# Kernel optimization log

Measured on AMD Instinct MI355X. Metric: run time of the kernel, lower is better.

The kernel has to match this reference:

```python
import jax, jax.numpy as jnp
import numpy as np
import math

V_ORDER = 22
N_ORDER = 22
HID = 128
MAX_ABS = 0.99
LOG_F0_MIN = math.log(80.0)
LOG_F0_MAX = math.log(1000.0)
OUT = 1 + V_ORDER + 1 + N_ORDER + 1 + HID  # 175


def setup_inputs() -> dict:
    key = jax.random.key(0)
    k1, k2, k3 = jax.random.split(key, 3)
    B, F, D = 32, 1000, 1024
    h = jax.random.normal(k1, (B, F, D), jnp.float32)
    W = jax.random.normal(k2, (OUT, D), jnp.float32) * 0.02
    b = jax.random.normal(k3, (OUT,), jnp.float32) * 0.1
    return {"h": h, "W": W, "b": b}


def _logits2biquads(logits):
    # conj representation: logits (..., 2) -> monic biquad coeffs (..., 3)
    mag = jax.nn.sigmoid(logits[..., 0]) * MAX_ABS
    phase = jax.nn.sigmoid(logits[..., 1]) * jnp.pi
    a1 = -2.0 * mag * jnp.cos(phase)
    a2 = mag * mag
    return jnp.stack([jnp.ones_like(a1), a1, a2], axis=-1)


def _biquads2lpc(biquads):
    # biquads: (..., S, 3) monic sections -> full LPC poly coeffs (..., 2S)
    # sequentially convolve the S second-order sections (b0 == 1 exactly)
    S = biquads.shape[-2]
    L = 2 * S + 1
    poly = jnp.zeros(biquads.shape[:-2] + (L,), biquads.dtype).at[..., 0].set(1.0)

    def shift(p, n):
        pad = [(0, 0)] * (p.ndim - 1) + [(n, 0)]
        return jnp.pad(p, pad)[..., :L]

    for i in range(S):  # small fixed S (=11), fully vectorized over batch/frames
        a1 = biquads[..., i, 1:2]
        a2 = biquads[..., i, 2:3]
        poly = poly + shift(poly, 1) * a1 + shift(poly, 2) * a2
    return poly[..., 1:]  # drop leading 1


def reference(h, W, b):
    B, F, _ = h.shape
    y = jnp.einsum('bfd,od->bfo', h, W) + b  # backbone out_linear
    idx = np.cumsum([1, V_ORDER, 1, N_ORDER, 1])
    f0_l, v_lpc_l, v_gain_l, n_lpc_l, n_gain_l, h_feat = jnp.split(y, idx, axis=-1)
    f0 = jnp.exp(jax.nn.sigmoid(f0_l[..., 0]) * (LOG_F0_MAX - LOG_F0_MIN) + LOG_F0_MIN)
    voice_lpc = _biquads2lpc(_logits2biquads(v_lpc_l.reshape(B, F, -1, 2)))
    noise_lpc = _biquads2lpc(_logits2biquads(n_lpc_l.reshape(B, F, -1, 2)))
    voice_gain = jnp.exp(v_gain_l[..., 0])
    noise_gain = jnp.exp(n_gain_l[..., 0])
    # flat version of (f0, (h,), (voice_gain, voice_lpc), (noise_gain, noise_lpc), ())
    return (f0, h_feat, voice_gain, voice_lpc, noise_gain, noise_lpc)
```

## Files before the change

### kernel.cpp

```cpp
#include <hip/hip_runtime.h>
#include <math.h>

#define D_DIM  1024
#define OUT_N  175
#define HID_N  128
#define BM     64
#define BK     32
#define NT     (D_DIM / BK)
#define LDK    40
#define NFRAG  11
#define FRAG_STRIDE 512

#define V_OFF   1
#define VG_OFF  23
#define N_OFF   24
#define NG_OFF  46
#define HF_OFF  47

#define LOG_F0_MIN 4.3820266346738812f
#define LOG_F0_MAX 6.9077552789821368f
#define PI_F       3.14159265358979323846f

typedef __attribute__((ext_vector_type(8))) short s16x8;
typedef __attribute__((ext_vector_type(4))) short s16x4;
typedef __attribute__((ext_vector_type(4))) float f32x4;

static __device__ __forceinline__ short f2bf(float f) {
    unsigned u = __float_as_uint(f);
    unsigned r = (u + 0x7fffu + ((u >> 16) & 1u)) >> 16;
    return (short)r;
}
static __device__ __forceinline__ float bf2f(short s) {
    return __uint_as_float(((unsigned)(unsigned short)s) << 16);
}

__global__ __launch_bounds__(64) void build_wfrag(
    const float* __restrict__ W, short* __restrict__ whiF, short* __restrict__ wloF)
{
    const int ft   = blockIdx.x;
    const int j    = ft >> 5;
    const int t    = ft & 31;
    const int lane = threadIdx.x;
    const int n    = 16 * j + (lane & 15);
    const int k    = 32 * t + (lane >> 4) * 8;

    float v[8];
    if (n < OUT_N) {
        float4 p0 = *(const float4*)(W + (size_t)n * D_DIM + k);
        float4 p1 = *(const float4*)(W + (size_t)n * D_DIM + k + 4);
        v[0] = p0.x; v[1] = p0.y; v[2] = p0.z; v[3] = p0.w;
        v[4] = p1.x; v[5] = p1.y; v[6] = p1.z; v[7] = p1.w;
    } else {
        #pragma unroll
        for (int e = 0; e < 8; ++e) v[e] = 0.f;
    }
    s16x8 hv, lv;
    #pragma unroll
    for (int e = 0; e < 8; ++e) {
        short hb = f2bf(v[e]);
        hv[e] = hb;
        lv[e] = f2bf(v[e] - bf2f(hb));
    }
    const size_t off = ((size_t)ft * 64 + lane) * 8;
    *(s16x8*)(whiF + off) = hv;
    *(s16x8*)(wloF + off) = lv;
}

#define SMEM_BYTES 12544

__global__ __launch_bounds__(512, 4) void glottal_main(
    const float* __restrict__ h, const short* __restrict__ whiF,
    const short* __restrict__ wloF, const float* __restrict__ bias,
    float* __restrict__ out, int R)
{
    __shared__ __align__(16) char smem[SMEM_BYTES];
    short* AhiS = (short*)smem;
    short* AloS = AhiS + BM * LDK;
    float (*yS)[49] = (float (*)[49])smem;

    const int tid  = threadIdx.x;
    const int r0   = blockIdx.x * BM;

    const int lane = tid & 63;
    const int wid  = tid >> 6;
    const int c    = lane & 15;
    const int kg   = lane >> 4;
    const int mh   = wid >> 2;
    const int jg   = wid & 3;
    const int jcnt = (jg < 3) ? 3 : 2;

    const int rA  = tid >> 3;
    const int kqA = (tid & 7) << 2;
    int gA = r0 + rA; if (gA >= R) gA = R - 1;
    const float* hP = h + (size_t)gA * D_DIM + kqA;

    const short* bhP[3];
    const short* blP[3];
    #pragma unroll
    for (int jj = 0; jj < 3; ++jj) {
        int j = 3 * jg + jj; if (j > NFRAG - 1) j = NFRAG - 1;
        bhP[jj] = whiF + (size_t)j * NT * FRAG_STRIDE + lane * 8;
        blP[jj] = wloF + (size_t)j * NT * FRAG_STRIDE + lane * 8;
    }

    f32x4 acc[2][3];
    #pragma unroll
    for (int mm = 0; mm < 2; ++mm)
        #pragma unroll
        for (int jj = 0; jj < 3; ++jj) acc[mm][jj] = f32x4{0.f, 0.f, 0.f, 0.f};

    float4 aC = *(const float4*)(hP);
    s16x8 bhC[3], blC[3];
    #pragma unroll
    for (int jj = 0; jj < 3; ++jj) if (jj < jcnt) {
        bhC[jj] = *(const s16x8*)(bhP[jj]);
        blC[jj] = *(const s16x8*)(blP[jj]);
    }

    for (int t = 0; t < NT; ++t) {
        {
            s16x4 hv, lv;
            hv.x = f2bf(aC.x); lv.x = f2bf(aC.x - bf2f(hv.x));
            hv.y = f2bf(aC.y); lv.y = f2bf(aC.y - bf2f(hv.y));
            hv.z = f2bf(aC.z); lv.z = f2bf(aC.z - bf2f(hv.z));
            hv.w = f2bf(aC.w); lv.w = f2bf(aC.w - bf2f(hv.w));
            *(s16x4*)(AhiS + rA * LDK + kqA) = hv;
            *(s16x4*)(AloS + rA * LDK + kqA) = lv;
        }
        __syncthreads();

        float4 aN;
        s16x8 bhN[3], blN[3];
        const bool more = (t + 1 < NT);
        if (more) {
            aN = *(const float4*)(hP + (t + 1) * BK);
            #pragma unroll
            for (int jj = 0; jj < 3; ++jj) if (jj < jcnt) {
                bhN[jj] = *(const s16x8*)(bhP[jj] + (size_t)(t + 1) * FRAG_STRIDE);
                blN[jj] = *(const s16x8*)(blP[jj] + (size_t)(t + 1) * FRAG_STRIDE);
            }
        }

        s16x8 ah[2], al[2];
        #pragma unroll
        for (int mm = 0; mm < 2; ++mm) {
            const int ro = (32 * mh + 16 * mm + c) * LDK + kg * 8;
            ah[mm] = *(const s16x8*)(AhiS + ro);
            al[mm] = *(const s16x8*)(AloS + ro);
        }

        #pragma unroll
        for (int jj = 0; jj < 3; ++jj) if (jj < jcnt) {
            #pragma unroll
            for (int mm = 0; mm < 2; ++mm) {
                acc[mm][jj] = __builtin_amdgcn_mfma_f32_16x16x32_bf16(ah[mm], bhC[jj], acc[mm][jj], 0, 0, 0);
                acc[mm][jj] = __builtin_amdgcn_mfma_f32_16x16x32_bf16(ah[mm], blC[jj], acc[mm][jj], 0, 0, 0);
                acc[mm][jj] = __builtin_amdgcn_mfma_f32_16x16x32_bf16(al[mm], bhC[jj], acc[mm][jj], 0, 0, 0);
            }
        }
        __syncthreads();

        if (more) {
            aC = aN;
            #pragma unroll
            for (int jj = 0; jj < 3; ++jj) if (jj < jcnt) {
                bhC[jj] = bhN[jj];
                blC[jj] = blN[jj];
            }
        }
    }

    const size_t Rz = (size_t)R;

    #pragma unroll
    for (int jj = 0; jj < 3; ++jj) if (jj < jcnt) {
        const int j   = 3 * jg + jj;
        const int col = 16 * j + c;
        const float bb = (col < OUT_N) ? bias[col] : 0.f;
        #pragma unroll
        for (int mm = 0; mm < 2; ++mm) {
            const int rb = 32 * mh + 16 * mm + (kg << 2);
            if (col >= HF_OFF && col < OUT_N) {
                #pragma unroll
                for (int r = 0; r < 4; ++r) {
                    int gr = r0 + rb + r;
                    if (gr < R)
                        out[Rz + (size_t)gr * HID_N + (col - HF_OFF)] = acc[mm][jj][r] + bb;
                }
            } else if (col < HF_OFF) {
                #pragma unroll
                for (int r = 0; r < 4; ++r)
                    yS[rb + r][col] = acc[mm][jj][r] + bb;
            }
        }
    }
    __syncthreads();

    if (tid < 2 * BM) {
        const int rr   = tid >> 1;
        const int half = tid & 1;
        const int gr   = r0 + rr;
        if (gr < R) {
            const float* yrow = yS[rr];

            if (half == 0) {
                float s = 1.f / (1.f + expf(-yrow[0]));
                out[gr] = expf(s * (LOG_F0_MAX - LOG_F0_MIN) + LOG_F0_MIN);
            }

            const int lbase = half ? N_OFF  : V_OFF;
            const int gidx  = half ? NG_OFF : VG_OFF;
            float*    gout  = out + (half ? Rz * 152 : Rz * 129);
            float*    lout  = out + (half ? Rz * 153 : Rz * 130);

            gout[gr] = expf(yrow[gidx]);

            float poly[23];
            poly[0] = 1.f;
            #pragma unroll
            for (int j = 1; j < 23; ++j) poly[j] = 0.f;

            #pragma unroll
            for (int i = 0; i < 11; ++i) {
                float l0  = yrow[lbase + 2 * i];
                float l1  = yrow[lbase + 2 * i + 1];
                float mag = 0.99f / (1.f + expf(-l0));
                float ph  = PI_F   / (1.f + expf(-l1));
                float a1  = -2.f * mag * cosf(ph);
                float a2  = mag * mag;
                #pragma unroll
                for (int j = 22; j >= 2; --j)
                    poly[j] = fmaf(a1, poly[j - 1], fmaf(a2, poly[j - 2], poly[j]));
                poly[1] = fmaf(a1, poly[0], poly[1]);
            }

            #pragma unroll
            for (int j = 0; j < 22; ++j)
                lout[(size_t)gr * 22 + j] = poly[j + 1];
        }
    }
}

extern "C" void kernel_launch(void* const* d_in, const int* in_sizes, int n_in,
                              void* d_out, int out_size, void* d_ws, size_t ws_size,
                              hipStream_t stream) {
    const float* h    = (const float*)d_in[0];
    const float* W    = (const float*)d_in[1];
    const float* bias = (const float*)d_in[2];
    float* out        = (float*)d_out;

    const int R = in_sizes[0] / D_DIM;
    const int blocks = (R + BM - 1) / BM;

    short* whiF = (short*)d_ws;
    short* wloF = whiF + (size_t)NFRAG * NT * FRAG_STRIDE;

    build_wfrag<<<NFRAG * NT, 64, 0, stream>>>(W, whiF, wloF);
    glottal_main<<<blocks, 512, 0, stream>>>(h, whiF, wloF, bias, out, R);
}
```

Before: 226.2 us.

## Stage 128-wide K chunks with register prefetch and fewer waves per block

The main GEMM kernel now runs 4 waves per block instead of 8. Each wave covers all 64 rows for its column fragments, so every W fragment loaded is reused across four M tiles. The activation tile is staged in LDS as 128-wide K chunks (four 32-wide sub-tiles), and the next chunk is prefetched into registers one chunk ahead. This cuts barriers from two per 32-wide K step to two per 128-wide chunk and halves W fragment traffic per block. In exchange each thread holds more registers (12 accumulators and 8 prefetched float4s), LDS use per block rises, and fewer waves are resident per CU.

```diff
diff --git a/kernel.cpp b/kernel.cpp
--- a/kernel.cpp
+++ b/kernel.cpp
@@ -5,11 +5,13 @@
 #define OUT_N  175
 #define HID_N  128
 #define BM     64
-#define BK     32
-#define NT     (D_DIM / BK)
-#define LDK    40
+#define NT     32
 #define NFRAG  11
 #define FRAG_STRIDE 512
+#define CH     128
+#define NCH    (D_DIM / CH)
+#define TPC    4
+#define SUBT   2576
 
 #define V_OFF   1
 #define VG_OFF  23
@@ -66,16 +68,16 @@
     *(s16x8*)(wloF + off) = lv;
 }
 
-#define SMEM_BYTES 12544
-
-__global__ __launch_bounds__(512, 4) void glottal_main(
+#define SMEM_BYTES (2 * TPC * SUBT * 2)
+
+__global__ __launch_bounds__(256, 2) void glottal_main(
     const float* __restrict__ h, const short* __restrict__ whiF,
     const short* __restrict__ wloF, const float* __restrict__ bias,
     float* __restrict__ out, int R)
 {
     __shared__ __align__(16) char smem[SMEM_BYTES];
     short* AhiS = (short*)smem;
-    short* AloS = AhiS + BM * LDK;
+    short* AloS = AhiS + TPC * SUBT;
     float (*yS)[49] = (float (*)[49])smem;
 
     const int tid  = threadIdx.x;
@@ -85,14 +87,13 @@
     const int wid  = tid >> 6;
     const int c    = lane & 15;
     const int kg   = lane >> 4;
-    const int mh   = wid >> 2;
-    const int jg   = wid & 3;
+    const int jg   = wid;
     const int jcnt = (jg < 3) ? 3 : 2;
 
-    const int rA  = tid >> 3;
-    const int kqA = (tid & 7) << 2;
-    int gA = r0 + rA; if (gA >= R) gA = R - 1;
-    const float* hP = h + (size_t)gA * D_DIM + kqA;
+    const int srow = tid >> 5;
+    const int scf  = tid & 31;
+    const int st4  = scf >> 3;
+    const int sko  = (scf & 7) << 2;
 
     const short* bhP[3];
     const short* blP[3];
@@ -103,70 +104,99 @@
         blP[jj] = wloF + (size_t)j * NT * FRAG_STRIDE + lane * 8;
     }
 
-    f32x4 acc[2][3];
-    #pragma unroll
-    for (int mm = 0; mm < 2; ++mm)
+    f32x4 acc[4][3];
+    #pragma unroll
+    for (int mm = 0; mm < 4; ++mm)
         #pragma unroll
         for (int jj = 0; jj < 3; ++jj) acc[mm][jj] = f32x4{0.f, 0.f, 0.f, 0.f};
 
-    float4 aC = *(const float4*)(hP);
-    s16x8 bhC[3], blC[3];
-    #pragma unroll
-    for (int jj = 0; jj < 3; ++jj) if (jj < jcnt) {
-        bhC[jj] = *(const s16x8*)(bhP[jj]);
-        blC[jj] = *(const s16x8*)(blP[jj]);
-    }
-
-    for (int t = 0; t < NT; ++t) {
-        {
-            s16x4 hv, lv;
-            hv.x = f2bf(aC.x); lv.x = f2bf(aC.x - bf2f(hv.x));
-            hv.y = f2bf(aC.y); lv.y = f2bf(aC.y - bf2f(hv.y));
-            hv.z = f2bf(aC.z); lv.z = f2bf(aC.z - bf2f(hv.z));
-            hv.w = f2bf(aC.w); lv.w = f2bf(aC.w - bf2f(hv.w));
-            *(s16x4*)(AhiS + rA * LDK + kqA) = hv;
-            *(s16x4*)(AloS + rA * LDK + kqA) = lv;
+    const float* hP[8];
+    #pragma unroll
+    for (int i = 0; i < 8; ++i) {
+        int gr = r0 + srow + 8 * i; if (gr >= R) gr = R - 1;
+        hP[i] = h + (size_t)gr * D_DIM + scf * 4;
+    }
+
+    float4 sA[8];
+
+    #pragma unroll
+    for (int i = 0; i < 8; ++i) sA[i] = *(const float4*)(hP[i]);
+    #pragma unroll
+    for (int i = 0; i < 8; ++i) {
+        const int base = st4 * SUBT + (srow + 8 * i) * 40 + sko;
+        s16x4 hv, lv;
+        hv.x = f2bf(sA[i].x); lv.x = f2bf(sA[i].x - bf2f(hv.x));
+        hv.y = f2bf(sA[i].y); lv.y = f2bf(sA[i].y - bf2f(hv.y));
+        hv.z = f2bf(sA[i].z); lv.z = f2bf(sA[i].z - bf2f(hv.z));
+        hv.w = f2bf(sA[i].w); lv.w = f2bf(sA[i].w - bf2f(hv.w));
+        *(s16x4*)(AhiS + base) = hv;
+        *(s16x4*)(AloS + base) = lv;
+    }
+    #pragma unroll
+    for (int i = 0; i < 8; ++i) sA[i] = *(const float4*)(hP[i] + CH);
+    __syncthreads();
+
+    for (int ch = 0; ch < NCH; ++ch) {
+        s16x8 bhC[3], blC[3];
+        const int tg0 = ch * TPC;
+        #pragma unroll
+        for (int jj = 0; jj < 3; ++jj) if (jj < jcnt) {
+            bhC[jj] = *(const s16x8*)(bhP[jj] + (size_t)tg0 * FRAG_STRIDE);
+            blC[jj] = *(const s16x8*)(blP[jj] + (size_t)tg0 * FRAG_STRIDE);
+        }
+        #pragma unroll
+        for (int t4 = 0; t4 < TPC; ++t4) {
+            s16x8 ah[4], al[4];
+            #pragma unroll
+            for (int mm = 0; mm < 4; ++mm) {
+                const int off = t4 * SUBT + (16 * mm + c) * 40 + kg * 8;
+                ah[mm] = *(const s16x8*)(AhiS + off);
+                al[mm] = *(const s16x8*)(AloS + off);
+            }
+            s16x8 bhN[3], blN[3];
+            if (t4 < TPC - 1) {
+                #pragma unroll
+                for (int jj = 0; jj < 3; ++jj) if (jj < jcnt) {
+                    bhN[jj] = *(const s16x8*)(bhP[jj] + (size_t)(tg0 + t4 + 1) * FRAG_STRIDE);
+                    blN[jj] = *(const s16x8*)(blP[jj] + (size_t)(tg0 + t4 + 1) * FRAG_STRIDE);
+                }
+            }
+            #pragma unroll
+            for (int jj = 0; jj < 3; ++jj) if (jj < jcnt) {
+                #pragma unroll
+                for (int mm = 0; mm < 4; ++mm) {
+                    acc[mm][jj] = __builtin_amdgcn_mfma_f32_16x16x32_bf16(ah[mm], bhC[jj], acc[mm][jj], 0, 0, 0);
+                    acc[mm][jj] = __builtin_amdgcn_mfma_f32_16x16x32_bf16(ah[mm], blC[jj], acc[mm][jj], 0, 0, 0);
+                    acc[mm][jj] = __builtin_amdgcn_mfma_f32_16x16x32_bf16(al[mm], bhC[jj], acc[mm][jj], 0, 0, 0);
+                }
+            }
+            if (t4 < TPC - 1) {
+                #pragma unroll
+                for (int jj = 0; jj < 3; ++jj) if (jj < jcnt) {
+                    bhC[jj] = bhN[jj]; blC[jj] = blN[jj];
+                }
+            }
         }
         __syncthreads();
 
-        float4 aN;
-        s16x8 bhN[3], blN[3];
-        const bool more = (t + 1 < NT);
-        if (more) {
-            aN = *(const float4*)(hP + (t + 1) * BK);
-            #pragma unroll
-            for (int jj = 0; jj < 3; ++jj) if (jj < jcnt) {
-                bhN[jj] = *(const s16x8*)(bhP[jj] + (size_t)(t + 1) * FRAG_STRIDE);
-                blN[jj] = *(const s16x8*)(blP[jj] + (size_t)(t + 1) * FRAG_STRIDE);
-            }
-        }
-
-        s16x8 ah[2], al[2];
-        #pragma unroll
-        for (int mm = 0; mm < 2; ++mm) {
-            const int ro = (32 * mh + 16 * mm + c) * LDK + kg * 8;
-            ah[mm] = *(const s16x8*)(AhiS + ro);
-            al[mm] = *(const s16x8*)(AloS + ro);
-        }
-
-        #pragma unroll
-        for (int jj = 0; jj < 3; ++jj) if (jj < jcnt) {
-            #pragma unroll
-            for (int mm = 0; mm < 2; ++mm) {
-                acc[mm][jj] = __builtin_amdgcn_mfma_f32_16x16x32_bf16(ah[mm], bhC[jj], acc[mm][jj], 0, 0, 0);
-                acc[mm][jj] = __builtin_amdgcn_mfma_f32_16x16x32_bf16(ah[mm], blC[jj], acc[mm][jj], 0, 0, 0);
-                acc[mm][jj] = __builtin_amdgcn_mfma_f32_16x16x32_bf16(al[mm], bhC[jj], acc[mm][jj], 0, 0, 0);
-            }
-        }
-        __syncthreads();
-
-        if (more) {
-            aC = aN;
-            #pragma unroll
-            for (int jj = 0; jj < 3; ++jj) if (jj < jcnt) {
-                bhC[jj] = bhN[jj];
-                blC[jj] = blN[jj];
-            }
+        if (ch < NCH - 1) {
+            #pragma unroll
+            for (int i = 0; i < 8; ++i) {
+                const int base = st4 * SUBT + (srow + 8 * i) * 40 + sko;
+                s16x4 hv, lv;
+                hv.x = f2bf(sA[i].x); lv.x = f2bf(sA[i].x - bf2f(hv.x));
+                hv.y = f2bf(sA[i].y); lv.y = f2bf(sA[i].y - bf2f(hv.y));
+                hv.z = f2bf(sA[i].z); lv.z = f2bf(sA[i].z - bf2f(hv.z));
+                hv.w = f2bf(sA[i].w); lv.w = f2bf(sA[i].w - bf2f(hv.w));
+                *(s16x4*)(AhiS + base) = hv;
+                *(s16x4*)(AloS + base) = lv;
+            }
+            if (ch < NCH - 2) {
+                #pragma unroll
+                for (int i = 0; i < 8; ++i)
+                    sA[i] = *(const float4*)(hP[i] + (size_t)(ch + 2) * CH);
+            }
+            __syncthreads();
         }
     }
 
@@ -178,8 +208,8 @@
         const int col = 16 * j + c;
         const float bb = (col < OUT_N) ? bias[col] : 0.f;
         #pragma unroll
-        for (int mm = 0; mm < 2; ++mm) {
-            const int rb = 32 * mh + 16 * mm + (kg << 2);
+        for (int mm = 0; mm < 4; ++mm) {
+            const int rb = 16 * mm + (kg << 2);
             if (col >= HF_OFF && col < OUT_N) {
                 #pragma unroll
                 for (int r = 0; r < 4; ++r) {
@@ -256,5 +286,5 @@
     short* wloF = whiF + (size_t)NFRAG * NT * FRAG_STRIDE;
 
     build_wfrag<<<NFRAG * NT, 64, 0, stream>>>(W, whiF, wloF);
-    glottal_main<<<blocks, 512, 0, stream>>>(h, whiF, wloF, bias, out, R);
-}
+    glottal_main<<<blocks, 256, 0, stream>>>(h, whiF, wloF, bias, out, R);
+}
```

Result: faster. 215.0 us (-5.0%).

## Load A fragments directly from global into registers, drop LDS staging

Applied to the files above, without the earlier changes.

Each warp now loads its own h rows straight from global memory in MFMA fragment layout and splits them into bf16 hi/lo in registers. This removes the per-K-step LDS write/read and both __syncthreads barriers. Blocks shrink to 256 threads, with each warp covering all 64 rows for its column group. The cost is that every h row is read by four warps, so global/L2 traffic for h goes up, and register pressure rises from the 4x3 accumulators and the double-buffered A registers.

```diff
diff --git a/kernel.cpp b/kernel.cpp
--- a/kernel.cpp
+++ b/kernel.cpp
@@ -5,9 +5,7 @@
 #define OUT_N  175
 #define HID_N  128
 #define BM     64
-#define BK     32
-#define NT     (D_DIM / BK)
-#define LDK    40
+#define NT     32
 #define NFRAG  11
 #define FRAG_STRIDE 512
 
@@ -66,17 +64,12 @@
     *(s16x8*)(wloF + off) = lv;
 }
 
-#define SMEM_BYTES 12544
-
-__global__ __launch_bounds__(512, 4) void glottal_main(
+__global__ __launch_bounds__(256) void glottal_main(
     const float* __restrict__ h, const short* __restrict__ whiF,
     const short* __restrict__ wloF, const float* __restrict__ bias,
     float* __restrict__ out, int R)
 {
-    __shared__ __align__(16) char smem[SMEM_BYTES];
-    short* AhiS = (short*)smem;
-    short* AloS = AhiS + BM * LDK;
-    float (*yS)[49] = (float (*)[49])smem;
+    __shared__ float yS[64][49];
 
     const int tid  = threadIdx.x;
     const int r0   = blockIdx.x * BM;
@@ -85,14 +78,15 @@
     const int wid  = tid >> 6;
     const int c    = lane & 15;
     const int kg   = lane >> 4;
-    const int mh   = wid >> 2;
-    const int jg   = wid & 3;
+    const int jg   = wid;
     const int jcnt = (jg < 3) ? 3 : 2;
 
-    const int rA  = tid >> 3;
-    const int kqA = (tid & 7) << 2;
-    int gA = r0 + rA; if (gA >= R) gA = R - 1;
-    const float* hP = h + (size_t)gA * D_DIM + kqA;
+    const float* aRow[4];
+    #pragma unroll
+    for (int mm = 0; mm < 4; ++mm) {
+        int gr = r0 + 16 * mm + c; if (gr >= R) gr = R - 1;
+        aRow[mm] = h + (size_t)gr * D_DIM + kg * 8;
+    }
 
     const short* bhP[3];
     const short* blP[3];
@@ -103,37 +97,36 @@
         blP[jj] = wloF + (size_t)j * NT * FRAG_STRIDE + lane * 8;
     }
 
-    f32x4 acc[2][3];
-    #pragma unroll
-    for (int mm = 0; mm < 2; ++mm)
+    f32x4 acc[4][3];
+    #pragma unroll
+    for (int mm = 0; mm < 4; ++mm)
         #pragma unroll
         for (int jj = 0; jj < 3; ++jj) acc[mm][jj] = f32x4{0.f, 0.f, 0.f, 0.f};
 
-    float4 aC = *(const float4*)(hP);
-    s16x8 bhC[3], blC[3];
+    float4 aC[4][2];
+    s16x8  bhC[3], blC[3];
+    #pragma unroll
+    for (int mm = 0; mm < 4; ++mm) {
+        aC[mm][0] = *(const float4*)(aRow[mm]);
+        aC[mm][1] = *(const float4*)(aRow[mm] + 4);
+    }
     #pragma unroll
     for (int jj = 0; jj < 3; ++jj) if (jj < jcnt) {
         bhC[jj] = *(const s16x8*)(bhP[jj]);
         blC[jj] = *(const s16x8*)(blP[jj]);
     }
 
+    #pragma unroll 2
     for (int t = 0; t < NT; ++t) {
-        {
-            s16x4 hv, lv;
-            hv.x = f2bf(aC.x); lv.x = f2bf(aC.x - bf2f(hv.x));
-            hv.y = f2bf(aC.y); lv.y = f2bf(aC.y - bf2f(hv.y));
-            hv.z = f2bf(aC.z); lv.z = f2bf(aC.z - bf2f(hv.z));
-            hv.w = f2bf(aC.w); lv.w = f2bf(aC.w - bf2f(hv.w));
-            *(s16x4*)(AhiS + rA * LDK + kqA) = hv;
-            *(s16x4*)(AloS + rA * LDK + kqA) = lv;
-        }
-        __syncthreads();
-
-        float4 aN;
-        s16x8 bhN[3], blN[3];
+        float4 aN[4][2];
+        s16x8  bhN[3], blN[3];
         const bool more = (t + 1 < NT);
         if (more) {
-            aN = *(const float4*)(hP + (t + 1) * BK);
+            #pragma unroll
+            for (int mm = 0; mm < 4; ++mm) {
+                aN[mm][0] = *(const float4*)(aRow[mm] + (t + 1) * 32);
+                aN[mm][1] = *(const float4*)(aRow[mm] + (t + 1) * 32 + 4);
+            }
             #pragma unroll
             for (int jj = 0; jj < 3; ++jj) if (jj < jcnt) {
                 bhN[jj] = *(const s16x8*)(bhP[jj] + (size_t)(t + 1) * FRAG_STRIDE);
@@ -141,27 +134,35 @@
             }
         }
 
-        s16x8 ah[2], al[2];
-        #pragma unroll
-        for (int mm = 0; mm < 2; ++mm) {
-            const int ro = (32 * mh + 16 * mm + c) * LDK + kg * 8;
-            ah[mm] = *(const s16x8*)(AhiS + ro);
-            al[mm] = *(const s16x8*)(AloS + ro);
-        }
-
-        #pragma unroll
-        for (int jj = 0; jj < 3; ++jj) if (jj < jcnt) {
-            #pragma unroll
-            for (int mm = 0; mm < 2; ++mm) {
-                acc[mm][jj] = __builtin_amdgcn_mfma_f32_16x16x32_bf16(ah[mm], bhC[jj], acc[mm][jj], 0, 0, 0);
-                acc[mm][jj] = __builtin_amdgcn_mfma_f32_16x16x32_bf16(ah[mm], blC[jj], acc[mm][jj], 0, 0, 0);
-                acc[mm][jj] = __builtin_amdgcn_mfma_f32_16x16x32_bf16(al[mm], bhC[jj], acc[mm][jj], 0, 0, 0);
-            }
-        }
-        __syncthreads();
+        #pragma unroll
+        for (int mm = 0; mm < 4; ++mm) {
+            s16x8 ah, al;
+            {
+                float v;
+                short hb;
+                v = aC[mm][0].x; hb = f2bf(v); ah[0] = hb; al[0] = f2bf(v - bf2f(hb));
+                v = aC[mm][0].y; hb = f2bf(v); ah[1] = hb; al[1] = f2bf(v - bf2f(hb));
+                v = aC[mm][0].z; hb = f2bf(v); ah[2] = hb; al[2] = f2bf(v - bf2f(hb));
+                v = aC[mm][0].w; hb = f2bf(v); ah[3] = hb; al[3] = f2bf(v - bf2f(hb));
+                v = aC[mm][1].x; hb = f2bf(v); ah[4] = hb; al[4] = f2bf(v - bf2f(hb));
+                v = aC[mm][1].y; hb = f2bf(v); ah[5] = hb; al[5] = f2bf(v - bf2f(hb));
+                v = aC[mm][1].z; hb = f2bf(v); ah[6] = hb; al[6] = f2bf(v - bf2f(hb));
+                v = aC[mm][1].w; hb = f2bf(v); ah[7] = hb; al[7] = f2bf(v - bf2f(hb));
+            }
+            #pragma unroll
+            for (int jj = 0; jj < 3; ++jj) if (jj < jcnt) {
+                acc[mm][jj] = __builtin_amdgcn_mfma_f32_16x16x32_bf16(ah, bhC[jj], acc[mm][jj], 0, 0, 0);
+                acc[mm][jj] = __builtin_amdgcn_mfma_f32_16x16x32_bf16(ah, blC[jj], acc[mm][jj], 0, 0, 0);
+                acc[mm][jj] = __builtin_amdgcn_mfma_f32_16x16x32_bf16(al, bhC[jj], acc[mm][jj], 0, 0, 0);
+            }
+        }
 
         if (more) {
-            aC = aN;
+            #pragma unroll
+            for (int mm = 0; mm < 4; ++mm) {
+                aC[mm][0] = aN[mm][0];
+                aC[mm][1] = aN[mm][1];
+            }
             #pragma unroll
             for (int jj = 0; jj < 3; ++jj) if (jj < jcnt) {
                 bhC[jj] = bhN[jj];
@@ -178,8 +179,8 @@
         const int col = 16 * j + c;
         const float bb = (col < OUT_N) ? bias[col] : 0.f;
         #pragma unroll
-        for (int mm = 0; mm < 2; ++mm) {
-            const int rb = 32 * mh + 16 * mm + (kg << 2);
+        for (int mm = 0; mm < 4; ++mm) {
+            const int rb = 16 * mm + (kg << 2);
             if (col >= HF_OFF && col < OUT_N) {
                 #pragma unroll
                 for (int r = 0; r < 4; ++r) {
@@ -256,5 +257,5 @@
     short* wloF = whiF + (size_t)NFRAG * NT * FRAG_STRIDE;
 
     build_wfrag<<<NFRAG * NT, 64, 0, stream>>>(W, whiF, wloF);
-    glottal_main<<<blocks, 512, 0, stream>>>(h, whiF, wloF, bias, out, R);
-}
+    glottal_main<<<blocks, 256, 0, stream>>>(h, whiF, wloF, bias, out, R);
+}
```

New measurement: 248.9 us. 1.1x slower.
